# Optimization experiments

Hardware: AMD Instinct MI355X
Metric: run time of the kernel (lower is better)

## Reference

```python
import jax, jax.numpy as jnp
import numpy as np

EPS_LN = 1e-5


def _ln(x, g, b):
    m = jnp.mean(x, axis=-1, keepdims=True)
    v = jnp.var(x, axis=-1, keepdims=True)
    return (x - m) * jax.lax.rsqrt(v + EPS_LN) * g + b


def setup_inputs() -> dict:
    B, T, D, DV, NV, DS = 8, 2048, 128, 32, 64, 16
    key = jax.random.key(0)
    ks = jax.random.split(key, 24)
    s = 0.02
    inp = {
        'x_head': jax.random.normal(ks[0], (B, T, D), jnp.float32),
        'gate': jax.random.uniform(ks[1], (B, T, 1), jnp.float32),
        'mask': jnp.zeros((1, T, T), jnp.float32),
        'node_bias_6d': jax.random.normal(ks[2], (6,), jnp.float32),
        'vertex_emb': jax.random.normal(ks[3], (NV, DV), jnp.float32),
        'adj_bias': jax.random.normal(ks[4], (NV, NV), jnp.float32),
        'spectral_emb': jax.random.normal(ks[5], (NV, DS), jnp.float32),
        'fractal_W_spec_weight': jax.random.normal(ks[6], (DV, DS), jnp.float32),
        # learned params (torch Linear weight is [out, in])
        'cn_g': jnp.ones((D,), jnp.float32), 'cn_b': jnp.zeros((D,), jnp.float32),
        'Wq': jax.random.normal(ks[7], (D, D), jnp.float32) * s,
        'Wk': jax.random.normal(ks[8], (D, D), jnp.float32) * s,
        'Wv': jax.random.normal(ks[9], (D, D), jnp.float32) * s,
        'bn_g': jnp.ones((D,), jnp.float32), 'bn_b': jnp.zeros((D,), jnp.float32),
        'Wg_w': jax.random.normal(ks[10], (6, D), jnp.float32) * s,
        'Wg_b': jnp.zeros((6,), jnp.float32),
        'g2v': jax.random.normal(ks[11], (DV, 6), jnp.float32) * s,
        'v2h': jax.random.normal(ks[12], (D, DV), jnp.float32) * s,
        'pc_w': jax.random.normal(ks[13], (D, 2 * D), jnp.float32) * s,
        'pc_b': jnp.zeros((D,), jnp.float32),
        'pn_g': jnp.ones((D,), jnp.float32), 'pn_b': jnp.zeros((D,), jnp.float32),
        'pu_w': jax.random.normal(ks[14], (2 * D, D), jnp.float32) * s,
        'pu_b': jnp.zeros((2 * D,), jnp.float32),
        'pd_w': jax.random.normal(ks[15], (D, 2 * D), jnp.float32) * s,
        'pd_b': jnp.zeros((D,), jnp.float32),
    }
    return inp


def reference(x_head, gate, mask, node_bias_6d, vertex_emb, adj_bias, spectral_emb,
              fractal_W_spec_weight, cn_g, cn_b, Wq, Wk, Wv, bn_g, bn_b, Wg_w, Wg_b,
              g2v, v2h, pc_w, pc_b, pn_g, pn_b, pu_w, pu_b, pd_w, pd_b):
    d_head = x_head.shape[-1]
    scale = jnp.asarray(np.sqrt(d_head), jnp.float32)

    # --- center: gated attention (scores in fp32) ---
    h = _ln(x_head, cn_g, cn_b)
    Q = (h @ Wq.T) * gate
    K = (h @ Wk.T) * gate
    V = h @ Wv.T
    scores = jnp.einsum('btd,bsd->bts', Q.astype(jnp.float32), K.astype(jnp.float32)) / scale
    scores = scores + mask
    alignment = scores  # head_index == 0
    attn = jax.nn.softmax(scores, axis=-1).astype(x_head.dtype)
    center_out = jnp.einsum('bts,bsd->btd', attn, V)
    center_signal = x_head + center_out

    # --- boundary: hypercube vertex routing with top-8 straight-through ---
    h_b = _ln(x_head, bn_g, bn_b)
    gates_6d = jax.nn.sigmoid(h_b @ Wg_w.T + Wg_b + node_bias_6d)      # [B,T,6]
    gate_proj = gates_6d @ g2v.T                                       # [B,T,DV]
    v_scores = gate_proj @ vertex_emb.T                                # [B,T,NV]
    spec_proj = spectral_emb @ fractal_W_spec_weight.T                 # [NV,DV]
    v_scores = v_scores + 0.1 * (gate_proj @ spec_proj.T)
    v_scores = v_scores + 0.1 * (v_scores @ adj_bias)

    mean_abs = jax.lax.stop_gradient(jnp.maximum(jnp.mean(jnp.abs(v_scores)), 1e-6))
    v32 = (v_scores / mean_abs).astype(jnp.float32) * 3.0
    soft_pi = jax.nn.softmax(v32, axis=-1)                             # [B,T,NV]
    topk_vals, topk_idx = jax.lax.top_k(soft_pi, 8)                    # [B,T,8]
    nv = soft_pi.shape[-1]
    hard_pi = jnp.sum(jax.nn.one_hot(topk_idx, nv, dtype=soft_pi.dtype) * topk_vals[..., None], axis=-2)
    hard_pi = hard_pi / (jnp.sum(hard_pi, axis=-1, keepdims=True) + 1e-8)
    pi = (hard_pi - jax.lax.stop_gradient(soft_pi) + soft_pi).astype(x_head.dtype)

    vertex_ctx = pi @ vertex_emb                                       # [B,T,DV]
    boundary_signal = x_head + vertex_ctx @ v2h.T

    # --- field: gated FFN over combined signal ---
    phi_input = jnp.concatenate([center_signal, boundary_signal], axis=-1) @ pc_w.T + pc_b
    phi_h = _ln(phi_input, pn_g, pn_b)
    phi_out = jax.nn.gelu(phi_h @ pu_w.T + pu_b, approximate=False) @ pd_w.T + pd_b
    field_output = phi_input + phi_out
    return (field_output, pi, alignment)
```

## Files before the change

kernel.cpp:

```cpp
#include <hip/hip_runtime.h>
#include <cmath>

typedef __bf16 bf16_t;
typedef bf16_t bf16x8 __attribute__((ext_vector_type(8)));
typedef bf16_t bf16x4 __attribute__((ext_vector_type(4)));
typedef float f32x4 __attribute__((ext_vector_type(4)));

#define DEVI static __device__ __forceinline__

constexpr int TB = 8;
constexpr int TT = 2048;
constexpr int BT_ = TB * TT;
constexpr float EPS_LN = 1e-5f;

DEVI f32x4 mfma16(bf16x8 a, bf16x8 b, f32x4 c) {
  return __builtin_amdgcn_mfma_f32_16x16x32_bf16(a, b, c, 0, 0, 0);
}

DEVI bf16x8 cvt8(float4 a, float4 b) {
  bf16x8 v;
  v[0] = (bf16_t)a.x; v[1] = (bf16_t)a.y; v[2] = (bf16_t)a.z; v[3] = (bf16_t)a.w;
  v[4] = (bf16_t)b.x; v[5] = (bf16_t)b.y; v[6] = (bf16_t)b.z; v[7] = (bf16_t)b.w;
  return v;
}

DEVI void gload_lds16(const void* g, void* l) {
  __builtin_amdgcn_global_load_lds(
      (const __attribute__((address_space(1))) unsigned int*)g,
      (__attribute__((address_space(3))) unsigned int*)l, 16, 0, 0);
}

__global__ __launch_bounds__(256) void k_prep(
    const float* __restrict__ Wq, const float* __restrict__ Wk,
    const float* __restrict__ Wv, const float* __restrict__ Wpc,
    const float* __restrict__ Wpu, const float* __restrict__ Wpd,
    bf16_t* __restrict__ wf) {
  int g = blockIdx.x * 256 + threadIdx.x;
  const float* W;
  bf16_t* dst;
  int rel, lks, Kdim;
  if (g < 6144) {
    int m = g >> 11; rel = g & 2047;
    W = (m == 0) ? Wq : ((m == 1) ? Wk : Wv);
    dst = wf + m * 16384; lks = 2; Kdim = 128;
  } else if (g < 10240) {
    rel = g - 6144; W = Wpc; dst = wf + 49152; lks = 3; Kdim = 256;
  } else if (g < 14336) {
    rel = g - 10240; W = Wpu; dst = wf + 81920; lks = 2; Kdim = 128;
  } else {
    rel = g - 14336; W = Wpd; dst = wf + 114688; lks = 3; Kdim = 256;
  }
  int lane = rel & 63;
  int fk = (rel >> 6) & ((1 << lks) - 1);
  int n0 = rel >> (6 + lks);
  int row = n0 * 16 + (lane & 15);
  int col = fk * 32 + (lane >> 4) * 8;
  const float* s = W + row * Kdim + col;
  float4 a = *(const float4*)s;
  float4 b = *(const float4*)(s + 4);
  *(bf16x8*)(dst + (size_t)rel * 8) = cvt8(a, b);
}

__global__ __launch_bounds__(256) void k_qkv(
    const float* __restrict__ x, const float* __restrict__ gate,
    const float* __restrict__ cn_g, const float* __restrict__ cn_b,
    const bf16_t* __restrict__ wf,
    bf16_t* __restrict__ Qo, bf16_t* __restrict__ Ko, bf16_t* __restrict__ Vt) {
  __shared__ __align__(16) bf16_t sH[64 * 128];
  const int tid = threadIdx.x;
  const int sel = blockIdx.x >> 8;
  const int t0 = (blockIdx.x & 255) * 64;

  {
    const int tok = tid >> 2, part = tid & 3;
    const float* xr = x + (size_t)(t0 + tok) * 128 + part * 32;
    float v[32];
    float s0 = 0.f, s1 = 0.f;
#pragma unroll
    for (int i = 0; i < 8; ++i) {
      float4 f = ((const float4*)xr)[i];
      v[i * 4 + 0] = f.x; v[i * 4 + 1] = f.y; v[i * 4 + 2] = f.z; v[i * 4 + 3] = f.w;
      s0 += f.x + f.y + f.z + f.w;
      s1 += f.x * f.x + f.y * f.y + f.z * f.z + f.w * f.w;
    }
    s0 += __shfl_xor(s0, 1); s0 += __shfl_xor(s0, 2);
    s1 += __shfl_xor(s1, 1); s1 += __shfl_xor(s1, 2);
    float mean = s0 * (1.f / 128.f);
    float var = s1 * (1.f / 128.f) - mean * mean;
    float rstd = rsqrtf(var + EPS_LN);
#pragma unroll
    for (int j8 = 0; j8 < 4; ++j8) {
      bf16x8 hv;
#pragma unroll
      for (int k = 0; k < 8; ++k) {
        int d = part * 32 + j8 * 8 + k;
        float hn = (v[j8 * 8 + k] - mean) * rstd;
        hv[k] = (bf16_t)(hn * cn_g[d] + cn_b[d]);
      }
      int bl = part * 4 + j8;
      *(bf16x8*)(&sH[tok * 128 + ((bl ^ (tok & 7)) * 8)]) = hv;
    }
  }
  __syncthreads();

  const int wave = tid >> 6, lane = tid & 63;
  const int rt = lane & 15, kg = lane >> 4;
  const int arow = wave * 16 + rt;
  bf16x8 af[4];
#pragma unroll
  for (int ks = 0; ks < 4; ++ks)
    af[ks] = *(const bf16x8*)(&sH[arow * 128 + (((ks * 4 + kg) ^ (rt & 7)) * 8)]);

  const int trow0 = t0 + wave * 16 + kg * 4;
  float4 g4 = *(const float4*)(gate + trow0);
  float gr[4] = {g4.x, g4.y, g4.z, g4.w};
  const int b_ = trow0 >> 11;
  const int tloc = trow0 & 2047;

  {
    const bf16_t* wm = wf + sel * 16384;
    bf16_t* O = sel ? Ko : Qo;
#pragma unroll
    for (int n0 = 0; n0 < 8; ++n0) {
      f32x4 acc = {0.f, 0.f, 0.f, 0.f};
#pragma unroll
      for (int ks = 0; ks < 4; ++ks) {
        bf16x8 bf = *(const bf16x8*)(wm + ((size_t)(n0 * 4 + ks) * 64 + lane) * 8);
        acc = mfma16(af[ks], bf, acc);
      }
#pragma unroll
      for (int r = 0; r < 4; ++r)
        O[(size_t)(trow0 + r) * 128 + n0 * 16 + rt] = (bf16_t)(acc[r] * gr[r]);
    }
  }
  {
    const bf16_t* wv = wf + 2 * 16384;
#pragma unroll
    for (int n0h = 0; n0h < 4; ++n0h) {
      int n0 = sel * 4 + n0h;
      f32x4 acc = {0.f, 0.f, 0.f, 0.f};
#pragma unroll
      for (int ks = 0; ks < 4; ++ks) {
        bf16x8 bf = *(const bf16x8*)(wv + ((size_t)(n0 * 4 + ks) * 64 + lane) * 8);
        acc = mfma16(af[ks], bf, acc);
      }
      bf16x4 pk;
      pk[0] = (bf16_t)acc[0]; pk[1] = (bf16_t)acc[1];
      pk[2] = (bf16_t)acc[2]; pk[3] = (bf16_t)acc[3];
      *(bf16x4*)(Vt + ((size_t)(b_ * 128 + n0 * 16 + rt)) * 2048 + tloc) = pk;
    }
  }
}

__global__ __launch_bounds__(256) void k_vscores(
    const float* __restrict__ x, const float* __restrict__ bn_g,
    const float* __restrict__ bn_b, const float* __restrict__ Wg_w,
    const float* __restrict__ Wg_b, const float* __restrict__ nb6,
    const float* __restrict__ g2v, const float* __restrict__ vemb,
    const float* __restrict__ adj, const float* __restrict__ spec,
    const float* __restrict__ wspec,
    float* __restrict__ vs_out, float* __restrict__ psum) {
  __shared__ float sWg[768];
  __shared__ float sG2V[192];
  __shared__ float sVE[64 * 33];
  __shared__ float sSP[64 * 33];
  __shared__ float sADJ[64 * 64];
  __shared__ float sRaw[64 * 68];
  __shared__ float sBN[256];
  __shared__ float bsum;
  const int tid = threadIdx.x;
  const int t0 = blockIdx.x * 64;
  if (tid == 0) bsum = 0.f;
  for (int i = tid; i < 768; i += 256) sWg[i] = Wg_w[i];
  for (int i = tid; i < 192; i += 256) sG2V[i] = g2v[i];
  for (int i = tid; i < 256; i += 256) sBN[i] = (i < 128) ? bn_g[i] : bn_b[i - 128];
  for (int i = tid; i < 2048; i += 256) sVE[(i >> 5) * 33 + (i & 31)] = vemb[i];
  for (int i = tid; i < 4096; i += 256) sADJ[i] = adj[i];
  for (int i = tid; i < 2048; i += 256) {
    int s = i >> 5, vv = i & 31;
    float acc = 0.f;
#pragma unroll
    for (int e = 0; e < 16; ++e) acc += spec[s * 16 + e] * wspec[vv * 16 + e];
    sSP[s * 33 + vv] = acc;
  }
  __syncthreads();

  const int tok = tid >> 2, part = tid & 3;
  const float* xr = x + (size_t)(t0 + tok) * 128 + part * 32;
  float v[32];
  float s0 = 0.f, s1 = 0.f;
#pragma unroll
  for (int i = 0; i < 8; ++i) {
    float4 f = ((const float4*)xr)[i];
    v[i * 4 + 0] = f.x; v[i * 4 + 1] = f.y; v[i * 4 + 2] = f.z; v[i * 4 + 3] = f.w;
    s0 += f.x + f.y + f.z + f.w;
    s1 += f.x * f.x + f.y * f.y + f.z * f.z + f.w * f.w;
  }
  s0 += __shfl_xor(s0, 1); s0 += __shfl_xor(s0, 2);
  s1 += __shfl_xor(s1, 1); s1 += __shfl_xor(s1, 2);
  float mean = s0 * (1.f / 128.f);
  float rstd = rsqrtf(s1 * (1.f / 128.f) - mean * mean + EPS_LN);
  float hb[32];
#pragma unroll
  for (int k = 0; k < 32; ++k) {
    int d = part * 32 + k;
    hb[k] = (v[k] - mean) * rstd * sBN[d] + sBN[128 + d];
  }
  float g6[6];
#pragma unroll
  for (int j = 0; j < 6; ++j) {
    float a = 0.f;
#pragma unroll
    for (int k = 0; k < 32; ++k) a += hb[k] * sWg[j * 128 + part * 32 + k];
    a += __shfl_xor(a, 1); a += __shfl_xor(a, 2);
    a += Wg_b[j] + nb6[j];
    g6[j] = 1.f / (1.f + __expf(-a));
  }
  float gp[32];
#pragma unroll
  for (int vv = 0; vv < 32; ++vv) {
    float a = 0.f;
#pragma unroll
    for (int j = 0; j < 6; ++j) a += g6[j] * sG2V[vv * 6 + j];
    gp[vv] = a;
  }
#pragma unroll
  for (int j = 0; j < 16; ++j) {
    int s = part * 16 + j;
    float a = 0.f;
#pragma unroll
    for (int vv = 0; vv < 32; ++vv)
      a += gp[vv] * (sVE[s * 33 + vv] + 0.1f * sSP[s * 33 + vv]);
    sRaw[tok * 68 + s] = a;
  }
  __syncthreads();

  float fin[16];
#pragma unroll
  for (int j = 0; j < 16; ++j) fin[j] = 0.f;
  for (int s = 0; s < 64; ++s) {
    float rv = sRaw[tok * 68 + s];
#pragma unroll
    for (int j = 0; j < 16; ++j) fin[j] += rv * sADJ[s * 64 + part * 16 + j];
  }
  float sa = 0.f;
#pragma unroll
  for (int j = 0; j < 16; ++j) {
    fin[j] = sRaw[tok * 68 + part * 16 + j] + 0.1f * fin[j];
    sa += fabsf(fin[j]);
  }
  float* o = vs_out + (size_t)(t0 + tok) * 64 + part * 16;
#pragma unroll
  for (int j4 = 0; j4 < 4; ++j4) {
    float4 f;
    f.x = fin[j4 * 4 + 0]; f.y = fin[j4 * 4 + 1];
    f.z = fin[j4 * 4 + 2]; f.w = fin[j4 * 4 + 3];
    ((float4*)o)[j4] = f;
  }
#pragma unroll
  for (int m = 1; m <= 32; m <<= 1) sa += __shfl_xor(sa, m);
  if ((tid & 63) == 0) atomicAdd(&bsum, sa);
  __syncthreads();
  if (tid == 0) psum[blockIdx.x] = bsum;
}

__global__ __launch_bounds__(256) void k_attn(
    const bf16_t* __restrict__ Q, const bf16_t* __restrict__ Kp,
    const bf16_t* __restrict__ Vt, const float* __restrict__ x,
    const float* __restrict__ mask, float* __restrict__ align_out,
    bf16_t* __restrict__ center, float* __restrict__ o_part,
    float* __restrict__ ml_part, int nsplit) {
  __shared__ __align__(16) bf16_t sK[2][64 * 128];
  __shared__ __align__(16) bf16_t sV[2][128 * 64];
  __shared__ __align__(16) bf16_t sP[4][16 * 72];
  const int tid = threadIdx.x;
  const int b_ = blockIdx.x & 7;
  const int qt = (blockIdx.x >> 3) & 31;
  const int sq = blockIdx.x >> 8;
  const int ntile = 32 / nsplit;
  const int st0 = sq * ntile;
  const int wave = tid >> 6, lane = tid & 63;
  const int rt = lane & 15, kg = lane >> 4;
  const size_t tq0 = (size_t)b_ * TT + qt * 64;

  bf16x8 qf[4];
#pragma unroll
  for (int ks = 0; ks < 4; ++ks)
    qf[ks] = *(const bf16x8*)(Q + (tq0 + wave * 16 + rt) * 128 + ks * 32 + kg * 8);

  f32x4 o[8];
  f32x4 zero4 = {0.f, 0.f, 0.f, 0.f};
#pragma unroll
  for (int i = 0; i < 8; ++i) o[i] = zero4;
  float m[4], l[4];
#pragma unroll
  for (int r = 0; r < 4; ++r) { m[r] = -INFINITY; l[r] = 0.f; }
  const float inv_sc = 0.08838834764831845f;
  const int tqr = qt * 64 + wave * 16 + kg * 4;
  const int koff = wave * 1024 + lane * 16;

  auto stage = [&](int buf, int st) {
    const int sb2 = st * 64;
#pragma unroll
    for (int i = 0; i < 4; ++i) {
      int off = i * 4096 + koff;
      int row = off >> 8;
      int c16 = (off >> 4) & 15;
      const char* src = (const char*)Kp +
          ((size_t)(b_ * TT + sb2 + row) * 128 + ((c16 ^ (row & 7)) * 8)) * 2;
      gload_lds16(src, (char*)(&sK[buf][0]) + i * 4096 + wave * 1024);
    }
#pragma unroll
    for (int i = 0; i < 4; ++i) {
      int off = i * 4096 + koff;
      int row = off >> 7;
      int c16 = (off >> 4) & 7;
      const char* src = (const char*)Vt +
          ((size_t)(b_ * 128 + row) * 2048 + sb2 + ((c16 ^ (row & 7)) * 8)) * 2;
      gload_lds16(src, (char*)(&sV[buf][0]) + i * 4096 + wave * 1024);
    }
  };

  stage(0, st0);
  for (int it = 0; it < ntile; ++it) {
    const int cur = it & 1;
    const int sb = (st0 + it) * 64;

    float mreg[4][4];
#pragma unroll
    for (int ct = 0; ct < 4; ++ct) {
      const int scol = sb + ct * 16 + rt;
#pragma unroll
      for (int r = 0; r < 4; ++r)
        mreg[ct][r] = mask[(size_t)(tqr + r) * TT + scol];
    }

    asm volatile("s_waitcnt vmcnt(16)" ::: "memory");
    __builtin_amdgcn_sched_barrier(0);
    __builtin_amdgcn_s_barrier();
    stage(cur ^ 1, (it + 1 < ntile) ? (st0 + it + 1) : (st0 + it));

    float p[4][4];
#pragma unroll
    for (int ct = 0; ct < 4; ++ct) {
      const int brow = ct * 16 + rt;
      f32x4 acc = zero4;
#pragma unroll
      for (int ks = 0; ks < 4; ++ks) {
        bf16x8 kf = *(const bf16x8*)(&sK[cur][brow * 128 + (((ks * 4 + kg) ^ (rt & 7)) * 8)]);
        acc = mfma16(qf[ks], kf, acc);
      }
      p[ct][0] = acc[0]; p[ct][1] = acc[1]; p[ct][2] = acc[2]; p[ct][3] = acc[3];
    }

    asm volatile("s_waitcnt vmcnt(8)" ::: "memory");
    __builtin_amdgcn_sched_barrier(0);

#pragma unroll
    for (int ct = 0; ct < 4; ++ct) {
      const int scol = sb + ct * 16 + rt;
#pragma unroll
      for (int r = 0; r < 4; ++r) {
        float sv = p[ct][r] * inv_sc + mreg[ct][r];
        align_out[((size_t)b_ * TT + tqr + r) * TT + scol] = sv;
        p[ct][r] = sv;
      }
    }
    float mn[4], fsc[4];
#pragma unroll
    for (int r = 0; r < 4; ++r) {
      float pm = fmaxf(fmaxf(p[0][r], p[1][r]), fmaxf(p[2][r], p[3][r]));
#pragma unroll
      for (int dm = 1; dm <= 8; dm <<= 1) pm = fmaxf(pm, __shfl_xor(pm, dm));
      mn[r] = fmaxf(m[r], pm);
      fsc[r] = __expf(m[r] - mn[r]);
      m[r] = mn[r];
    }
    float rs[4] = {0.f, 0.f, 0.f, 0.f};
#pragma unroll
    for (int ct = 0; ct < 4; ++ct)
#pragma unroll
      for (int r = 0; r < 4; ++r) {
        float pe = __expf(p[ct][r] - mn[r]);
        p[ct][r] = pe;
        rs[r] += pe;
      }
#pragma unroll
    for (int r = 0; r < 4; ++r) {
#pragma unroll
      for (int dm = 1; dm <= 8; dm <<= 1) rs[r] += __shfl_xor(rs[r], dm);
      l[r] = l[r] * fsc[r] + rs[r];
    }
#pragma unroll
    for (int i = 0; i < 8; ++i) {
      o[i][0] *= fsc[0]; o[i][1] *= fsc[1]; o[i][2] *= fsc[2]; o[i][3] *= fsc[3];
    }
#pragma unroll
    for (int ct = 0; ct < 4; ++ct)
#pragma unroll
      for (int r = 0; r < 4; ++r)
        sP[wave][(kg * 4 + r) * 72 + ct * 16 + rt] = (bf16_t)p[ct][r];
    asm volatile("" ::: "memory");
    bf16x8 pf[2];
#pragma unroll
    for (int ks = 0; ks < 2; ++ks)
      pf[ks] = *(const bf16x8*)(&sP[wave][rt * 72 + ks * 32 + kg * 8]);
#pragma unroll
    for (int n0 = 0; n0 < 8; ++n0) {
      const int brow = n0 * 16 + rt;
      f32x4 acc = o[n0];
#pragma unroll
      for (int ks = 0; ks < 2; ++ks) {
        bf16x8 vf = *(const bf16x8*)(&sV[cur][brow * 64 + (((ks * 4 + kg) ^ (rt & 7)) * 8)]);
        acc = mfma16(pf[ks], vf, acc);
      }
      o[n0] = acc;
    }
  }

  const size_t trow = tq0 + wave * 16 + kg * 4;
  if (nsplit == 1) {
    float il[4];
#pragma unroll
    for (int r = 0; r < 4; ++r) il[r] = 1.f / l[r];
#pragma unroll
    for (int n0 = 0; n0 < 8; ++n0) {
      int col = n0 * 16 + rt;
#pragma unroll
      for (int r = 0; r < 4; ++r) {
        float val = o[n0][r] * il[r] + x[(trow + r) * 128 + col];
        center[(trow + r) * 128 + col] = (bf16_t)val;
      }
    }
  } else {
#pragma unroll
    for (int n0 = 0; n0 < 8; ++n0) {
      int col = n0 * 16 + rt;
#pragma unroll
      for (int r = 0; r < 4; ++r)
        o_part[((size_t)sq * BT_ + trow + r) * 128 + col] = o[n0][r];
    }
    if (rt == 0) {
#pragma unroll
      for (int r = 0; r < 4; ++r) {
        size_t t = (size_t)sq * BT_ + trow + r;
        ml_part[t * 2] = m[r];
        ml_part[t * 2 + 1] = l[r];
      }
    }
  }
}

__global__ __launch_bounds__(256) void k_comb(
    const float* __restrict__ x, const float* __restrict__ o_part,
    const float* __restrict__ ml_part, bf16_t* __restrict__ center) {
  const int tid = threadIdx.x;
  const int tok = blockIdx.x * 64 + (tid >> 2);
  const int part = tid & 3;
  float m0 = ml_part[(size_t)tok * 2];
  float l0 = ml_part[(size_t)tok * 2 + 1];
  float m1 = ml_part[((size_t)BT_ + tok) * 2];
  float l1 = ml_part[((size_t)BT_ + tok) * 2 + 1];
  float M = fmaxf(m0, m1);
  float w0 = __expf(m0 - M), w1 = __expf(m1 - M);
  float inv = 1.f / (l0 * w0 + l1 * w1);
  w0 *= inv; w1 *= inv;
  const float* xr = x + (size_t)tok * 128 + part * 32;
  const float* o0 = o_part + (size_t)tok * 128 + part * 32;
  const float* o1 = o_part + ((size_t)BT_ + tok) * 128 + part * 32;
  bf16_t* cr = center + (size_t)tok * 128 + part * 32;
#pragma unroll
  for (int c = 0; c < 4; ++c) {
    float4 a0 = ((const float4*)(o0 + c * 8))[0];
    float4 b0 = ((const float4*)(o0 + c * 8))[1];
    float4 a1 = ((const float4*)(o1 + c * 8))[0];
    float4 b1 = ((const float4*)(o1 + c * 8))[1];
    float4 xa = ((const float4*)(xr + c * 8))[0];
    float4 xb = ((const float4*)(xr + c * 8))[1];
    bf16x8 ov;
    ov[0] = (bf16_t)(a0.x * w0 + a1.x * w1 + xa.x);
    ov[1] = (bf16_t)(a0.y * w0 + a1.y * w1 + xa.y);
    ov[2] = (bf16_t)(a0.z * w0 + a1.z * w1 + xa.z);
    ov[3] = (bf16_t)(a0.w * w0 + a1.w * w1 + xa.w);
    ov[4] = (bf16_t)(b0.x * w0 + b1.x * w1 + xb.x);
    ov[5] = (bf16_t)(b0.y * w0 + b1.y * w1 + xb.y);
    ov[6] = (bf16_t)(b0.z * w0 + b1.z * w1 + xb.z);
    ov[7] = (bf16_t)(b0.w * w0 + b1.w * w1 + xb.w);
    *(bf16x8*)(cr + c * 8) = ov;
  }
}

__global__ __launch_bounds__(256) void k_pi(
    const float* __restrict__ x, const float* __restrict__ vs,
    const float* __restrict__ psum, const float* __restrict__ vemb,
    const float* __restrict__ v2h,
    float* __restrict__ pi_out, bf16_t* __restrict__ bound) {
  __shared__ float red[256];
  __shared__ float sVE[64 * 33];
  __shared__ float sV2H[128 * 33];
  const int tid = threadIdx.x;
  const int t0 = blockIdx.x * 64;
  red[tid] = psum[tid];
  for (int i = tid; i < 2048; i += 256) sVE[(i >> 5) * 33 + (i & 31)] = vemb[i];
  for (int i = tid; i < 4096; i += 256) sV2H[(i >> 5) * 33 + (i & 31)] = v2h[i];
  __syncthreads();
#pragma unroll
  for (int s = 128; s > 0; s >>= 1) {
    if (tid < s) red[tid] += red[tid + s];
    __syncthreads();
  }
  float mean_abs = fmaxf(red[0] * (1.f / 1048576.f), 1e-6f);
  float s3 = 3.f / mean_abs;

  const int tok = tid >> 2, part = tid & 3;
  const int tg = t0 + tok;
  const float* vr = vs + (size_t)tg * 64 + part * 16;
  float lg[16];
  float mx = -INFINITY;
#pragma unroll
  for (int j4 = 0; j4 < 4; ++j4) {
    float4 f = ((const float4*)vr)[j4];
    lg[j4 * 4 + 0] = f.x * s3; lg[j4 * 4 + 1] = f.y * s3;
    lg[j4 * 4 + 2] = f.z * s3; lg[j4 * 4 + 3] = f.w * s3;
    mx = fmaxf(mx, fmaxf(fmaxf(lg[j4 * 4 + 0], lg[j4 * 4 + 1]),
                         fmaxf(lg[j4 * 4 + 2], lg[j4 * 4 + 3])));
  }
  mx = fmaxf(mx, __shfl_xor(mx, 1));
  mx = fmaxf(mx, __shfl_xor(mx, 2));
  float e[16];
  float tot = 0.f;
#pragma unroll
  for (int j = 0; j < 16; ++j) { e[j] = __expf(lg[j] - mx); tot += e[j]; }
  tot += __shfl_xor(tot, 1); tot += __shfl_xor(tot, 2);

  unsigned used = 0u;
  float tsum = 0.f;
#pragma unroll
  for (int it = 0; it < 8; ++it) {
    float bv = -INFINITY;
    int bi = 0;
#pragma unroll
    for (int j = 0; j < 16; ++j) {
      bool ok = !(used & (1u << j)) && (e[j] > bv);
      bv = ok ? e[j] : bv;
      bi = ok ? j : bi;
    }
    int gi = part * 16 + bi;
#pragma unroll
    for (int dm = 1; dm <= 2; dm <<= 1) {
      float ov = __shfl_xor(bv, dm);
      int oi = __shfl_xor(gi, dm);
      bool take = (ov > bv) || (ov == bv && oi < gi);
      bv = take ? ov : bv;
      gi = take ? oi : gi;
    }
    tsum += bv;
    if ((gi >> 4) == part) used |= 1u << (gi & 15);
  }
  float inv_tot = 1.f / tot;
  float inv_d = 1.f / (tsum * inv_tot + 1e-8f);
  float pi[16];
#pragma unroll
  for (int j = 0; j < 16; ++j)
    pi[j] = (used & (1u << j)) ? e[j] * inv_tot * inv_d : 0.f;
  float* po = pi_out + (size_t)tg * 64 + part * 16;
#pragma unroll
  for (int j4 = 0; j4 < 4; ++j4) {
    float4 f;
    f.x = pi[j4 * 4 + 0]; f.y = pi[j4 * 4 + 1];
    f.z = pi[j4 * 4 + 2]; f.w = pi[j4 * 4 + 3];
    ((float4*)po)[j4] = f;
  }
  float vc[32];
#pragma unroll
  for (int vv = 0; vv < 32; ++vv) vc[vv] = 0.f;
#pragma unroll
  for (int j = 0; j < 16; ++j) {
    float p = pi[j];
    int s = part * 16 + j;
#pragma unroll
    for (int vv = 0; vv < 32; ++vv) vc[vv] += p * sVE[s * 33 + vv];
  }
#pragma unroll
  for (int vv = 0; vv < 32; ++vv) {
    vc[vv] += __shfl_xor(vc[vv], 1);
    vc[vv] += __shfl_xor(vc[vv], 2);
  }
  const float* xr = x + (size_t)tg * 128 + part * 32;
  bf16_t* br = bound + (size_t)tg * 128 + part * 32;
#pragma unroll
  for (int d8 = 0; d8 < 4; ++d8) {
    float4 xa = ((const float4*)xr)[d8 * 2];
    float4 xb = ((const float4*)xr)[d8 * 2 + 1];
    float xv[8] = {xa.x, xa.y, xa.z, xa.w, xb.x, xb.y, xb.z, xb.w};
    bf16x8 ov;
#pragma unroll
    for (int k = 0; k < 8; ++k) {
      int d = part * 32 + d8 * 8 + k;
      float a = 0.f;
#pragma unroll
      for (int vv = 0; vv < 32; ++vv) a += vc[vv] * sV2H[d * 33 + vv];
      ov[k] = (bf16_t)(xv[k] + a);
    }
    *(bf16x8*)(br + d8 * 8) = ov;
  }
}

__global__ __launch_bounds__(256) void k_ffn(
    const bf16_t* __restrict__ center, const bf16_t* __restrict__ bound,
    const bf16_t* __restrict__ wf,
    const float* __restrict__ pc_b, const float* __restrict__ pn_g,
    const float* __restrict__ pn_b, const float* __restrict__ pu_b,
    const float* __restrict__ pd_b, float* __restrict__ out) {
  __shared__ __align__(16) bf16_t sH[32 * 128];
  __shared__ __align__(16) bf16_t sG[32 * 256];
  __shared__ float sLN[2][32][2];
  const bf16_t* wpc = wf + 49152;
  const bf16_t* wpu = wf + 81920;
  const bf16_t* wpd = wf + 114688;
  const int tid = threadIdx.x;
  const int t0 = blockIdx.x * 32;
  const int wave = tid >> 6, lane = tid & 63;
  const int g = wave & 1, h = wave >> 1;
  const int rt = lane & 15, kg = lane >> 4;
  const int arow = g * 16 + rt;

  bf16x8 af[8];
#pragma unroll
  for (int ks = 0; ks < 8; ++ks) {
    const bf16_t* src = (ks < 4)
        ? (center + (size_t)(t0 + arow) * 128 + ks * 32 + kg * 8)
        : (bound + (size_t)(t0 + arow) * 128 + (ks - 4) * 32 + kg * 8);
    af[ks] = *(const bf16x8*)src;
  }
  f32x4 phi[4];
#pragma unroll
  for (int j = 0; j < 4; ++j) {
    int n0 = 4 * h + j;
    f32x4 acc = {0.f, 0.f, 0.f, 0.f};
#pragma unroll
    for (int ks = 0; ks < 8; ++ks) {
      bf16x8 bf = *(const bf16x8*)(wpc + ((size_t)(n0 * 8 + ks) * 64 + lane) * 8);
      acc = mfma16(af[ks], bf, acc);
    }
    float bias = pc_b[n0 * 16 + rt];
    acc[0] += bias; acc[1] += bias; acc[2] += bias; acc[3] += bias;
    phi[j] = acc;
  }
#pragma unroll
  for (int r = 0; r < 4; ++r) {
    float s0 = 0.f, s1 = 0.f;
#pragma unroll
    for (int j = 0; j < 4; ++j) {
      float vv = phi[j][r];
      s0 += vv; s1 += vv * vv;
    }
#pragma unroll
    for (int dm = 1; dm <= 8; dm <<= 1) {
      s0 += __shfl_xor(s0, dm);
      s1 += __shfl_xor(s1, dm);
    }
    if (rt == 0) {
      int row = g * 16 + kg * 4 + r;
      sLN[h][row][0] = s0;
      sLN[h][row][1] = s1;
    }
  }
  __syncthreads();
  float mean[4], rstd[4];
#pragma unroll
  for (int r = 0; r < 4; ++r) {
    int row = g * 16 + kg * 4 + r;
    float s0 = sLN[0][row][0] + sLN[1][row][0];
    float s1 = sLN[0][row][1] + sLN[1][row][1];
    mean[r] = s0 * (1.f / 128.f);
    float var = s1 * (1.f / 128.f) - mean[r] * mean[r];
    rstd[r] = rsqrtf(var + EPS_LN);
  }
#pragma unroll
  for (int j = 0; j < 4; ++j) {
    int col = (4 * h + j) * 16 + rt;
    float gg = pn_g[col], bb = pn_b[col];
#pragma unroll
    for (int r = 0; r < 4; ++r) {
      float hv = (phi[j][r] - mean[r]) * rstd[r] * gg + bb;
      int row = g * 16 + kg * 4 + r;
      *(bf16_t*)((char*)sH + row * 256 + ((2 * col) ^ ((row & 7) << 4))) = (bf16_t)hv;
    }
  }
  __syncthreads();

  bf16x8 ah[4];
#pragma unroll
  for (int ks = 0; ks < 4; ++ks)
    ah[ks] = *(const bf16x8*)((const char*)sH + arow * 256 +
                              (((ks * 4 + kg) ^ (rt & 7)) * 16));
#pragma unroll
  for (int j2 = 0; j2 < 8; ++j2) {
    int n0 = 8 * h + j2;
    f32x4 acc = {0.f, 0.f, 0.f, 0.f};
#pragma unroll
    for (int ks = 0; ks < 4; ++ks) {
      bf16x8 bf = *(const bf16x8*)(wpu + ((size_t)(n0 * 4 + ks) * 64 + lane) * 8);
      acc = mfma16(ah[ks], bf, acc);
    }
    int col = n0 * 16 + rt;
    float bias = pu_b[col];
#pragma unroll
    for (int r = 0; r < 4; ++r) {
      float uv = acc[r] + bias;
      float gv = 0.5f * uv * (1.f + erff(uv * 0.7071067811865476f));
      int row = g * 16 + kg * 4 + r;
      *(bf16_t*)((char*)sG + row * 512 + ((2 * col) ^ ((row & 7) << 4))) = (bf16_t)gv;
    }
  }
  __syncthreads();

  bf16x8 ag[8];
#pragma unroll
  for (int ks = 0; ks < 8; ++ks)
    ag[ks] = *(const bf16x8*)((const char*)sG + arow * 512 +
                              (((ks * 4 + kg) ^ (rt & 7)) * 16));
#pragma unroll
  for (int j = 0; j < 4; ++j) {
    int n0 = 4 * h + j;
    f32x4 acc = {0.f, 0.f, 0.f, 0.f};
#pragma unroll
    for (int ks = 0; ks < 8; ++ks) {
      bf16x8 bf = *(const bf16x8*)(wpd + ((size_t)(n0 * 8 + ks) * 64 + lane) * 8);
      acc = mfma16(ag[ks], bf, acc);
    }
    float bias = pd_b[n0 * 16 + rt];
#pragma unroll
    for (int r = 0; r < 4; ++r) {
      int row = g * 16 + kg * 4 + r;
      out[(size_t)(t0 + row) * 128 + n0 * 16 + rt] = acc[r] + bias + phi[j][r];
    }
  }
}

extern "C" void kernel_launch(void* const* d_in, const int* in_sizes, int n_in,
                              void* d_out, int out_size, void* d_ws, size_t ws_size,
                              hipStream_t stream) {
  (void)in_sizes; (void)n_in; (void)out_size;
  const float* x     = (const float*)d_in[0];
  const float* gate  = (const float*)d_in[1];
  const float* mask  = (const float*)d_in[2];
  const float* nb6   = (const float*)d_in[3];
  const float* vemb  = (const float*)d_in[4];
  const float* adj   = (const float*)d_in[5];
  const float* spec  = (const float*)d_in[6];
  const float* wspec = (const float*)d_in[7];
  const float* cn_g  = (const float*)d_in[8];
  const float* cn_b  = (const float*)d_in[9];
  const float* Wq    = (const float*)d_in[10];
  const float* Wk    = (const float*)d_in[11];
  const float* Wv    = (const float*)d_in[12];
  const float* bn_g  = (const float*)d_in[13];
  const float* bn_b  = (const float*)d_in[14];
  const float* Wg_w  = (const float*)d_in[15];
  const float* Wg_b  = (const float*)d_in[16];
  const float* g2v   = (const float*)d_in[17];
  const float* v2h   = (const float*)d_in[18];
  const float* pc_w  = (const float*)d_in[19];
  const float* pc_b  = (const float*)d_in[20];
  const float* pn_g  = (const float*)d_in[21];
  const float* pn_b  = (const float*)d_in[22];
  const float* pu_w  = (const float*)d_in[23];
  const float* pu_b  = (const float*)d_in[24];
  const float* pd_w  = (const float*)d_in[25];
  const float* pd_b  = (const float*)d_in[26];

  char* ws = (char*)d_ws;
  bf16_t* Qb   = (bf16_t*)(ws);
  bf16_t* Kb   = (bf16_t*)(ws + (4u << 20));
  bf16_t* Vt   = (bf16_t*)(ws + (8u << 20));
  bf16_t* bnd  = (bf16_t*)(ws + (12u << 20));
  bf16_t* ctr  = (bf16_t*)(ws + (16u << 20));
  float*  vsc  = (float*)(ws + (20u << 20));
  float*  psum = (float*)(ws + (24u << 20));
  bf16_t* wfb  = (bf16_t*)(ws + (24u << 20) + 4096);
  float*  mlp  = (float*)(ws + (24u << 20) + (512u << 10));
  float*  opart= (float*)(ws + (25u << 20));

  const int nsplit = (ws_size >= ((size_t)41 << 20) + 65536) ? 2 : 1;

  float* f_out = (float*)d_out;
  float* pi_o  = f_out + (size_t)BT_ * 128;
  float* al_o  = pi_o + (size_t)BT_ * 64;

  k_prep<<<72, 256, 0, stream>>>(Wq, Wk, Wv, pc_w, pu_w, pd_w, wfb);
  k_qkv<<<512, 256, 0, stream>>>(x, gate, cn_g, cn_b, wfb, Qb, Kb, Vt);
  k_vscores<<<256, 256, 0, stream>>>(x, bn_g, bn_b, Wg_w, Wg_b, nb6, g2v, vemb,
                                     adj, spec, wspec, vsc, psum);
  k_attn<<<256 * nsplit, 256, 0, stream>>>(Qb, Kb, Vt, x, mask, al_o, ctr,
                                           opart, mlp, nsplit);
  if (nsplit == 2)
    k_comb<<<256, 256, 0, stream>>>(x, opart, mlp, ctr);
  k_pi<<<256, 256, 0, stream>>>(x, vsc, psum, vemb, v2h, pi_o, bnd);
  k_ffn<<<512, 256, 0, stream>>>(ctr, bnd, wfb, pc_b, pn_g, pn_b, pu_b, pd_b, f_out);
}
```

Before: 353.4 us.

## Merge small kernels, add nontemporal stores for big outputs, reorder qkv blocks

Merges the weight-prep kernel into the v-scores kernel, and the split-combine kernel into the pi kernel, as disjoint block ranges, cutting two launches. Makes the mask loads, the alignment-matrix stores and the FFN output stores nontemporal to reduce cache pollution from large streaming traffic. Remaps qkv block indices across batches and adds a scheduling barrier after staging in attention. The risk is that merged grids have uneven per-block work, and nontemporal hints may change write-combining behaviour.

```diff
diff --git a/kernel.cpp b/kernel.cpp
--- a/kernel.cpp
+++ b/kernel.cpp
@@ -30,129 +30,11 @@
       (__attribute__((address_space(3))) unsigned int*)l, 16, 0, 0);
 }
 
-__global__ __launch_bounds__(256) void k_prep(
+__global__ __launch_bounds__(256) void k_prep_vs(
     const float* __restrict__ Wq, const float* __restrict__ Wk,
     const float* __restrict__ Wv, const float* __restrict__ Wpc,
     const float* __restrict__ Wpu, const float* __restrict__ Wpd,
-    bf16_t* __restrict__ wf) {
-  int g = blockIdx.x * 256 + threadIdx.x;
-  const float* W;
-  bf16_t* dst;
-  int rel, lks, Kdim;
-  if (g < 6144) {
-    int m = g >> 11; rel = g & 2047;
-    W = (m == 0) ? Wq : ((m == 1) ? Wk : Wv);
-    dst = wf + m * 16384; lks = 2; Kdim = 128;
-  } else if (g < 10240) {
-    rel = g - 6144; W = Wpc; dst = wf + 49152; lks = 3; Kdim = 256;
-  } else if (g < 14336) {
-    rel = g - 10240; W = Wpu; dst = wf + 81920; lks = 2; Kdim = 128;
-  } else {
-    rel = g - 14336; W = Wpd; dst = wf + 114688; lks = 3; Kdim = 256;
-  }
-  int lane = rel & 63;
-  int fk = (rel >> 6) & ((1 << lks) - 1);
-  int n0 = rel >> (6 + lks);
-  int row = n0 * 16 + (lane & 15);
-  int col = fk * 32 + (lane >> 4) * 8;
-  const float* s = W + row * Kdim + col;
-  float4 a = *(const float4*)s;
-  float4 b = *(const float4*)(s + 4);
-  *(bf16x8*)(dst + (size_t)rel * 8) = cvt8(a, b);
-}
-
-__global__ __launch_bounds__(256) void k_qkv(
-    const float* __restrict__ x, const float* __restrict__ gate,
-    const float* __restrict__ cn_g, const float* __restrict__ cn_b,
-    const bf16_t* __restrict__ wf,
-    bf16_t* __restrict__ Qo, bf16_t* __restrict__ Ko, bf16_t* __restrict__ Vt) {
-  __shared__ __align__(16) bf16_t sH[64 * 128];
-  const int tid = threadIdx.x;
-  const int sel = blockIdx.x >> 8;
-  const int t0 = (blockIdx.x & 255) * 64;
-
-  {
-    const int tok = tid >> 2, part = tid & 3;
-    const float* xr = x + (size_t)(t0 + tok) * 128 + part * 32;
-    float v[32];
-    float s0 = 0.f, s1 = 0.f;
-#pragma unroll
-    for (int i = 0; i < 8; ++i) {
-      float4 f = ((const float4*)xr)[i];
-      v[i * 4 + 0] = f.x; v[i * 4 + 1] = f.y; v[i * 4 + 2] = f.z; v[i * 4 + 3] = f.w;
-      s0 += f.x + f.y + f.z + f.w;
-      s1 += f.x * f.x + f.y * f.y + f.z * f.z + f.w * f.w;
-    }
-    s0 += __shfl_xor(s0, 1); s0 += __shfl_xor(s0, 2);
-    s1 += __shfl_xor(s1, 1); s1 += __shfl_xor(s1, 2);
-    float mean = s0 * (1.f / 128.f);
-    float var = s1 * (1.f / 128.f) - mean * mean;
-    float rstd = rsqrtf(var + EPS_LN);
-#pragma unroll
-    for (int j8 = 0; j8 < 4; ++j8) {
-      bf16x8 hv;
-#pragma unroll
-      for (int k = 0; k < 8; ++k) {
-        int d = part * 32 + j8 * 8 + k;
-        float hn = (v[j8 * 8 + k] - mean) * rstd;
-        hv[k] = (bf16_t)(hn * cn_g[d] + cn_b[d]);
-      }
-      int bl = part * 4 + j8;
-      *(bf16x8*)(&sH[tok * 128 + ((bl ^ (tok & 7)) * 8)]) = hv;
-    }
-  }
-  __syncthreads();
-
-  const int wave = tid >> 6, lane = tid & 63;
-  const int rt = lane & 15, kg = lane >> 4;
-  const int arow = wave * 16 + rt;
-  bf16x8 af[4];
-#pragma unroll
-  for (int ks = 0; ks < 4; ++ks)
-    af[ks] = *(const bf16x8*)(&sH[arow * 128 + (((ks * 4 + kg) ^ (rt & 7)) * 8)]);
-
-  const int trow0 = t0 + wave * 16 + kg * 4;
-  float4 g4 = *(const float4*)(gate + trow0);
-  float gr[4] = {g4.x, g4.y, g4.z, g4.w};
-  const int b_ = trow0 >> 11;
-  const int tloc = trow0 & 2047;
-
-  {
-    const bf16_t* wm = wf + sel * 16384;
-    bf16_t* O = sel ? Ko : Qo;
-#pragma unroll
-    for (int n0 = 0; n0 < 8; ++n0) {
-      f32x4 acc = {0.f, 0.f, 0.f, 0.f};
-#pragma unroll
-      for (int ks = 0; ks < 4; ++ks) {
-        bf16x8 bf = *(const bf16x8*)(wm + ((size_t)(n0 * 4 + ks) * 64 + lane) * 8);
-        acc = mfma16(af[ks], bf, acc);
-      }
-#pragma unroll
-      for (int r = 0; r < 4; ++r)
-        O[(size_t)(trow0 + r) * 128 + n0 * 16 + rt] = (bf16_t)(acc[r] * gr[r]);
-    }
-  }
-  {
-    const bf16_t* wv = wf + 2 * 16384;
-#pragma unroll
-    for (int n0h = 0; n0h < 4; ++n0h) {
-      int n0 = sel * 4 + n0h;
-      f32x4 acc = {0.f, 0.f, 0.f, 0.f};
-#pragma unroll
-      for (int ks = 0; ks < 4; ++ks) {
-        bf16x8 bf = *(const bf16x8*)(wv + ((size_t)(n0 * 4 + ks) * 64 + lane) * 8);
-        acc = mfma16(af[ks], bf, acc);
-      }
-      bf16x4 pk;
-      pk[0] = (bf16_t)acc[0]; pk[1] = (bf16_t)acc[1];
-      pk[2] = (bf16_t)acc[2]; pk[3] = (bf16_t)acc[3];
-      *(bf16x4*)(Vt + ((size_t)(b_ * 128 + n0 * 16 + rt)) * 2048 + tloc) = pk;
-    }
-  }
-}
-
-__global__ __launch_bounds__(256) void k_vscores(
+    bf16_t* __restrict__ wf,
     const float* __restrict__ x, const float* __restrict__ bn_g,
     const float* __restrict__ bn_b, const float* __restrict__ Wg_w,
     const float* __restrict__ Wg_b, const float* __restrict__ nb6,
@@ -169,7 +51,36 @@
   __shared__ float sBN[256];
   __shared__ float bsum;
   const int tid = threadIdx.x;
-  const int t0 = blockIdx.x * 64;
+
+  if (blockIdx.x < 72) {
+    int g = blockIdx.x * 256 + tid;
+    const float* W;
+    bf16_t* dst;
+    int rel, lks, Kdim;
+    if (g < 6144) {
+      int m = g >> 11; rel = g & 2047;
+      W = (m == 0) ? Wq : ((m == 1) ? Wk : Wv);
+      dst = wf + m * 16384; lks = 2; Kdim = 128;
+    } else if (g < 10240) {
+      rel = g - 6144; W = Wpc; dst = wf + 49152; lks = 3; Kdim = 256;
+    } else if (g < 14336) {
+      rel = g - 10240; W = Wpu; dst = wf + 81920; lks = 2; Kdim = 128;
+    } else {
+      rel = g - 14336; W = Wpd; dst = wf + 114688; lks = 3; Kdim = 256;
+    }
+    int lane = rel & 63;
+    int fk = (rel >> 6) & ((1 << lks) - 1);
+    int n0 = rel >> (6 + lks);
+    int row = n0 * 16 + (lane & 15);
+    int col = fk * 32 + (lane >> 4) * 8;
+    const float* s = W + row * Kdim + col;
+    float4 a = *(const float4*)s;
+    float4 b = *(const float4*)(s + 4);
+    *(bf16x8*)(dst + (size_t)rel * 8) = cvt8(a, b);
+    return;
+  }
+
+  const int t0 = (blockIdx.x - 72) * 64;
   if (tid == 0) bsum = 0.f;
   for (int i = tid; i < 768; i += 256) sWg[i] = Wg_w[i];
   for (int i = tid; i < 192; i += 256) sG2V[i] = g2v[i];
@@ -261,7 +172,101 @@
   for (int m = 1; m <= 32; m <<= 1) sa += __shfl_xor(sa, m);
   if ((tid & 63) == 0) atomicAdd(&bsum, sa);
   __syncthreads();
-  if (tid == 0) psum[blockIdx.x] = bsum;
+  if (tid == 0) psum[blockIdx.x - 72] = bsum;
+}
+
+__global__ __launch_bounds__(256) void k_qkv(
+    const float* __restrict__ x, const float* __restrict__ gate,
+    const float* __restrict__ cn_g, const float* __restrict__ cn_b,
+    const bf16_t* __restrict__ wf,
+    bf16_t* __restrict__ Qo, bf16_t* __restrict__ Ko, bf16_t* __restrict__ Vt) {
+  __shared__ __align__(16) bf16_t sH[64 * 128];
+  const int tid = threadIdx.x;
+  const int sel = blockIdx.x >> 8;
+  const int g8 = blockIdx.x & 255;
+  const int bb = g8 & 7;
+  const int ii = g8 >> 3;
+  const int t0 = (bb * 32 + ii) * 64;
+
+  {
+    const int tok = tid >> 2, part = tid & 3;
+    const float* xr = x + (size_t)(t0 + tok) * 128 + part * 32;
+    float v[32];
+    float s0 = 0.f, s1 = 0.f;
+#pragma unroll
+    for (int i = 0; i < 8; ++i) {
+      float4 f = ((const float4*)xr)[i];
+      v[i * 4 + 0] = f.x; v[i * 4 + 1] = f.y; v[i * 4 + 2] = f.z; v[i * 4 + 3] = f.w;
+      s0 += f.x + f.y + f.z + f.w;
+      s1 += f.x * f.x + f.y * f.y + f.z * f.z + f.w * f.w;
+    }
+    s0 += __shfl_xor(s0, 1); s0 += __shfl_xor(s0, 2);
+    s1 += __shfl_xor(s1, 1); s1 += __shfl_xor(s1, 2);
+    float mean = s0 * (1.f / 128.f);
+    float var = s1 * (1.f / 128.f) - mean * mean;
+    float rstd = rsqrtf(var + EPS_LN);
+#pragma unroll
+    for (int j8 = 0; j8 < 4; ++j8) {
+      bf16x8 hv;
+#pragma unroll
+      for (int k = 0; k < 8; ++k) {
+        int d = part * 32 + j8 * 8 + k;
+        float hn = (v[j8 * 8 + k] - mean) * rstd;
+        hv[k] = (bf16_t)(hn * cn_g[d] + cn_b[d]);
+      }
+      int bl = part * 4 + j8;
+      *(bf16x8*)(&sH[tok * 128 + ((bl ^ (tok & 7)) * 8)]) = hv;
+    }
+  }
+  __syncthreads();
+
+  const int wave = tid >> 6, lane = tid & 63;
+  const int rt = lane & 15, kg = lane >> 4;
+  const int arow = wave * 16 + rt;
+  bf16x8 af[4];
+#pragma unroll
+  for (int ks = 0; ks < 4; ++ks)
+    af[ks] = *(const bf16x8*)(&sH[arow * 128 + (((ks * 4 + kg) ^ (rt & 7)) * 8)]);
+
+  const int trow0 = t0 + wave * 16 + kg * 4;
+  float4 g4 = *(const float4*)(gate + trow0);
+  float gr[4] = {g4.x, g4.y, g4.z, g4.w};
+  const int b_ = trow0 >> 11;
+  const int tloc = trow0 & 2047;
+
+  {
+    const bf16_t* wm = wf + sel * 16384;
+    bf16_t* O = sel ? Ko : Qo;
+#pragma unroll
+    for (int n0 = 0; n0 < 8; ++n0) {
+      f32x4 acc = {0.f, 0.f, 0.f, 0.f};
+#pragma unroll
+      for (int ks = 0; ks < 4; ++ks) {
+        bf16x8 bf = *(const bf16x8*)(wm + ((size_t)(n0 * 4 + ks) * 64 + lane) * 8);
+        acc = mfma16(af[ks], bf, acc);
+      }
+#pragma unroll
+      for (int r = 0; r < 4; ++r)
+        O[(size_t)(trow0 + r) * 128 + n0 * 16 + rt] = (bf16_t)(acc[r] * gr[r]);
+    }
+  }
+  {
+    const bf16_t* wv = wf + 2 * 16384;
+#pragma unroll
+    for (int n0h = 0; n0h < 4; ++n0h) {
+      int n0 = sel * 4 + n0h;
+      f32x4 acc = {0.f, 0.f, 0.f, 0.f};
+#pragma unroll
+      for (int ks = 0; ks < 4; ++ks) {
+        bf16x8 bf = *(const bf16x8*)(wv + ((size_t)(n0 * 4 + ks) * 64 + lane) * 8);
+        acc = mfma16(af[ks], bf, acc);
+      }
+      bf16x4 pk;
+      pk[0] = (bf16_t)acc[0]; pk[1] = (bf16_t)acc[1];
+      pk[2] = (bf16_t)acc[2]; pk[3] = (bf16_t)acc[3];
+      *(bf16x4*)(Vt + ((size_t)(b_ * 128 + n0 * 16 + rt)) * 2048 + tloc) = pk;
+    }
+  }
 }
 
 __global__ __launch_bounds__(256) void k_attn(
@@ -332,13 +337,15 @@
       const int scol = sb + ct * 16 + rt;
 #pragma unroll
       for (int r = 0; r < 4; ++r)
-        mreg[ct][r] = mask[(size_t)(tqr + r) * TT + scol];
+        mreg[ct][r] = __builtin_nontemporal_load(
+            mask + (size_t)(tqr + r) * TT + scol);
     }
 
     asm volatile("s_waitcnt vmcnt(16)" ::: "memory");
     __builtin_amdgcn_sched_barrier(0);
     __builtin_amdgcn_s_barrier();
     stage(cur ^ 1, (it + 1 < ntile) ? (st0 + it + 1) : (st0 + it));
+    __builtin_amdgcn_sched_barrier(0);
 
     float p[4][4];
 #pragma unroll
@@ -362,7 +369,8 @@
 #pragma unroll
       for (int r = 0; r < 4; ++r) {
         float sv = p[ct][r] * inv_sc + mreg[ct][r];
-        align_out[((size_t)b_ * TT + tqr + r) * TT + scol] = sv;
+        __builtin_nontemporal_store(
+            sv, align_out + ((size_t)b_ * TT + tqr + r) * TT + scol);
         p[ct][r] = sv;
       }
     }
@@ -451,55 +459,56 @@
   }
 }
 
-__global__ __launch_bounds__(256) void k_comb(
+__global__ __launch_bounds__(256) void k_comb_pi(
     const float* __restrict__ x, const float* __restrict__ o_part,
-    const float* __restrict__ ml_part, bf16_t* __restrict__ center) {
-  const int tid = threadIdx.x;
-  const int tok = blockIdx.x * 64 + (tid >> 2);
-  const int part = tid & 3;
-  float m0 = ml_part[(size_t)tok * 2];
-  float l0 = ml_part[(size_t)tok * 2 + 1];
-  float m1 = ml_part[((size_t)BT_ + tok) * 2];
-  float l1 = ml_part[((size_t)BT_ + tok) * 2 + 1];
-  float M = fmaxf(m0, m1);
-  float w0 = __expf(m0 - M), w1 = __expf(m1 - M);
-  float inv = 1.f / (l0 * w0 + l1 * w1);
-  w0 *= inv; w1 *= inv;
-  const float* xr = x + (size_t)tok * 128 + part * 32;
-  const float* o0 = o_part + (size_t)tok * 128 + part * 32;
-  const float* o1 = o_part + ((size_t)BT_ + tok) * 128 + part * 32;
-  bf16_t* cr = center + (size_t)tok * 128 + part * 32;
-#pragma unroll
-  for (int c = 0; c < 4; ++c) {
-    float4 a0 = ((const float4*)(o0 + c * 8))[0];
-    float4 b0 = ((const float4*)(o0 + c * 8))[1];
-    float4 a1 = ((const float4*)(o1 + c * 8))[0];
-    float4 b1 = ((const float4*)(o1 + c * 8))[1];
-    float4 xa = ((const float4*)(xr + c * 8))[0];
-    float4 xb = ((const float4*)(xr + c * 8))[1];
-    bf16x8 ov;
-    ov[0] = (bf16_t)(a0.x * w0 + a1.x * w1 + xa.x);
-    ov[1] = (bf16_t)(a0.y * w0 + a1.y * w1 + xa.y);
-    ov[2] = (bf16_t)(a0.z * w0 + a1.z * w1 + xa.z);
-    ov[3] = (bf16_t)(a0.w * w0 + a1.w * w1 + xa.w);
-    ov[4] = (bf16_t)(b0.x * w0 + b1.x * w1 + xb.x);
-    ov[5] = (bf16_t)(b0.y * w0 + b1.y * w1 + xb.y);
-    ov[6] = (bf16_t)(b0.z * w0 + b1.z * w1 + xb.z);
-    ov[7] = (bf16_t)(b0.w * w0 + b1.w * w1 + xb.w);
-    *(bf16x8*)(cr + c * 8) = ov;
-  }
-}
-
-__global__ __launch_bounds__(256) void k_pi(
-    const float* __restrict__ x, const float* __restrict__ vs,
-    const float* __restrict__ psum, const float* __restrict__ vemb,
-    const float* __restrict__ v2h,
-    float* __restrict__ pi_out, bf16_t* __restrict__ bound) {
+    const float* __restrict__ ml_part, bf16_t* __restrict__ center,
+    const float* __restrict__ vs, const float* __restrict__ psum,
+    const float* __restrict__ vemb, const float* __restrict__ v2h,
+    float* __restrict__ pi_out, bf16_t* __restrict__ bound, int nsplit) {
   __shared__ float red[256];
   __shared__ float sVE[64 * 33];
   __shared__ float sV2H[128 * 33];
   const int tid = threadIdx.x;
-  const int t0 = blockIdx.x * 64;
+
+  if (blockIdx.x < 256) {
+    if (nsplit == 1) return;
+    const int tok = blockIdx.x * 64 + (tid >> 2);
+    const int part = tid & 3;
+    float m0 = ml_part[(size_t)tok * 2];
+    float l0 = ml_part[(size_t)tok * 2 + 1];
+    float m1 = ml_part[((size_t)BT_ + tok) * 2];
+    float l1 = ml_part[((size_t)BT_ + tok) * 2 + 1];
+    float M = fmaxf(m0, m1);
+    float w0 = __expf(m0 - M), w1 = __expf(m1 - M);
+    float inv = 1.f / (l0 * w0 + l1 * w1);
+    w0 *= inv; w1 *= inv;
+    const float* xr = x + (size_t)tok * 128 + part * 32;
+    const float* o0 = o_part + (size_t)tok * 128 + part * 32;
+    const float* o1 = o_part + ((size_t)BT_ + tok) * 128 + part * 32;
+    bf16_t* cr = center + (size_t)tok * 128 + part * 32;
+#pragma unroll
+    for (int c = 0; c < 4; ++c) {
+      float4 a0 = ((const float4*)(o0 + c * 8))[0];
+      float4 b0 = ((const float4*)(o0 + c * 8))[1];
+      float4 a1 = ((const float4*)(o1 + c * 8))[0];
+      float4 b1 = ((const float4*)(o1 + c * 8))[1];
+      float4 xa = ((const float4*)(xr + c * 8))[0];
+      float4 xb = ((const float4*)(xr + c * 8))[1];
+      bf16x8 ov;
+      ov[0] = (bf16_t)(a0.x * w0 + a1.x * w1 + xa.x);
+      ov[1] = (bf16_t)(a0.y * w0 + a1.y * w1 + xa.y);
+      ov[2] = (bf16_t)(a0.z * w0 + a1.z * w1 + xa.z);
+      ov[3] = (bf16_t)(a0.w * w0 + a1.w * w1 + xa.w);
+      ov[4] = (bf16_t)(b0.x * w0 + b1.x * w1 + xb.x);
+      ov[5] = (bf16_t)(b0.y * w0 + b1.y * w1 + xb.y);
+      ov[6] = (bf16_t)(b0.z * w0 + b1.z * w1 + xb.z);
+      ov[7] = (bf16_t)(b0.w * w0 + b1.w * w1 + xb.w);
+      *(bf16x8*)(cr + c * 8) = ov;
+    }
+    return;
+  }
+
+  const int t0 = (blockIdx.x - 256) * 64;
   red[tid] = psum[tid];
   for (int i = tid; i < 2048; i += 256) sVE[(i >> 5) * 33 + (i & 31)] = vemb[i];
   for (int i = tid; i < 4096; i += 256) sV2H[(i >> 5) * 33 + (i & 31)] = v2h[i];
@@ -734,7 +743,9 @@
 #pragma unroll
     for (int r = 0; r < 4; ++r) {
       int row = g * 16 + kg * 4 + r;
-      out[(size_t)(t0 + row) * 128 + n0 * 16 + rt] = acc[r] + bias + phi[j][r];
+      __builtin_nontemporal_store(
+          acc[r] + bias + phi[j][r],
+          out + (size_t)(t0 + row) * 128 + n0 * 16 + rt);
     }
   }
 }
@@ -789,14 +800,13 @@
   float* pi_o  = f_out + (size_t)BT_ * 128;
   float* al_o  = pi_o + (size_t)BT_ * 64;
 
-  k_prep<<<72, 256, 0, stream>>>(Wq, Wk, Wv, pc_w, pu_w, pd_w, wfb);
+  k_prep_vs<<<328, 256, 0, stream>>>(Wq, Wk, Wv, pc_w, pu_w, pd_w, wfb,
+                                     x, bn_g, bn_b, Wg_w, Wg_b, nb6, g2v, vemb,
+                                     adj, spec, wspec, vsc, psum);
   k_qkv<<<512, 256, 0, stream>>>(x, gate, cn_g, cn_b, wfb, Qb, Kb, Vt);
-  k_vscores<<<256, 256, 0, stream>>>(x, bn_g, bn_b, Wg_w, Wg_b, nb6, g2v, vemb,
-                                     adj, spec, wspec, vsc, psum);
   k_attn<<<256 * nsplit, 256, 0, stream>>>(Qb, Kb, Vt, x, mask, al_o, ctr,
                                            opart, mlp, nsplit);
-  if (nsplit == 2)
-    k_comb<<<256, 256, 0, stream>>>(x, opart, mlp, ctr);
-  k_pi<<<256, 256, 0, stream>>>(x, vsc, psum, vemb, v2h, pi_o, bnd);
+  k_comb_pi<<<512, 256, 0, stream>>>(x, opart, mlp, ctr, vsc, psum, vemb, v2h,
+                                     pi_o, bnd, nsplit);
   k_ffn<<<512, 256, 0, stream>>>(ctr, bnd, wfb, pc_b, pn_g, pn_b, pu_b, pd_b, f_out);
 }
```

Measured after the change: 362.1 us. 2.5% more time.
